# Performance work log

Measured on AMD Instinct MI355X. Metric: run time of the kernel, lower is better.

Reference implementation:

```python
import jax, jax.numpy as jnp
import numpy as np

H = 2048       # hidden_size
NH = 16        # num query heads
NKV = 4        # num key/value heads
HD = 128       # head_dim
EPS = 1e-6
ROPE_BASE = 10000.0


def rms_norm(x, w):
    xf = x.astype(jnp.float32)
    var = jnp.mean(xf * xf, axis=-1, keepdims=True)
    return (w * (xf * jax.lax.rsqrt(var + EPS)).astype(x.dtype))


def rope_cos_sin(seq_len, dtype):
    inv_freq = 1.0 / (ROPE_BASE ** (jnp.arange(0, HD, 2, dtype=jnp.float32) / HD))
    pos = jnp.arange(seq_len, dtype=jnp.float32)
    ang = pos[:, None] * inv_freq[None, :]            # [S, HD/2]
    emb = jnp.concatenate([ang, ang], axis=-1)        # [S, HD]
    return jnp.cos(emb).astype(dtype), jnp.sin(emb).astype(dtype)


def rotate_half(x):
    x1, x2 = jnp.split(x, 2, axis=-1)
    return jnp.concatenate([-x2, x1], axis=-1)


def setup_inputs() -> dict:
    key = jax.random.key(0)
    ks = jax.random.split(key, 8)
    B, S = 2, 2048
    hidden_states = jax.random.normal(ks[0], (B, S, H), dtype=jnp.float32)
    # additive causal mask [B,1,S,S]
    causal = jnp.where(jnp.tril(jnp.ones((S, S), dtype=bool)), 0.0, -1e9).astype(jnp.float32)
    attention_mask = jnp.broadcast_to(causal[None, None], (B, 1, S, S))
    sc = 1.0 / np.sqrt(H)
    Wq = jax.random.normal(ks[1], (NH * HD, H), dtype=jnp.float32) * sc
    Wk = jax.random.normal(ks[2], (NKV * HD, H), dtype=jnp.float32) * sc
    Wv = jax.random.normal(ks[3], (NKV * HD, H), dtype=jnp.float32) * sc
    Wo = jax.random.normal(ks[4], (H, NH * HD), dtype=jnp.float32) * sc
    q_norm_w = jnp.ones((HD,), dtype=jnp.float32)
    k_norm_w = jnp.ones((HD,), dtype=jnp.float32)
    return {"hidden_states": hidden_states, "attention_mask": attention_mask,
            "Wq": Wq, "Wk": Wk, "Wv": Wv, "Wo": Wo,
            "q_norm_w": q_norm_w, "k_norm_w": k_norm_w}


def reference(hidden_states, attention_mask, Wq, Wk, Wv, Wo, q_norm_w, k_norm_w):
    B, S, _ = hidden_states.shape
    # projections (nn.Linear: x @ W.T)
    q = (hidden_states @ Wq.T).reshape(B, S, NH, HD).transpose(0, 2, 1, 3)   # [B,NH,S,HD]
    k = (hidden_states @ Wk.T).reshape(B, S, NKV, HD).transpose(0, 2, 1, 3)  # [B,NKV,S,HD]
    v = (hidden_states @ Wv.T).reshape(B, S, NKV, HD).transpose(0, 2, 1, 3)
    # QK RMSNorm over head_dim
    q = rms_norm(q, q_norm_w)
    k = rms_norm(k, k_norm_w)
    # RoPE
    cos, sin = rope_cos_sin(S, q.dtype)        # [S,HD]
    q = q * cos + rotate_half(q) * sin
    k = k * cos + rotate_half(k) * sin
    # GQA: repeat kv heads
    n_rep = NH // NKV
    k = jnp.repeat(k, n_rep, axis=1)           # [B,NH,S,HD]
    v = jnp.repeat(v, n_rep, axis=1)
    # attention
    scores = jnp.einsum('bhqd,bhkd->bhqk', q, k) / np.sqrt(HD)
    scores = scores + attention_mask
    probs = jax.nn.softmax(scores, axis=-1)
    attn = jnp.einsum('bhqk,bhkd->bhqd', probs, v)
    attn = attn.transpose(0, 2, 1, 3).reshape(B, S, NH * HD)
    return attn @ Wo.T
```

## Files before the change

kernel.cpp:

```cpp
#include <hip/hip_runtime.h>
#include <hip/hip_bf16.h>
#include <math.h>

#define NH 16
#define NKV 4
#define HD 128
#define SEQ 2048
#define BATCH 2
#define EPSF 1e-6f
#define QKV 3072

typedef __attribute__((ext_vector_type(8))) short bf16x8;
typedef __attribute__((ext_vector_type(4))) short short4v;
typedef __attribute__((ext_vector_type(4))) float f32x4;

__device__ __forceinline__ short f2bf(float x) {
    unsigned u = __float_as_uint(x);
    u += 0x7fffu + ((u >> 16) & 1u);
    return (short)(u >> 16);
}
__device__ __forceinline__ float bf2f(short x) {
    return __uint_as_float((unsigned)(unsigned short)x << 16);
}
__device__ __forceinline__ unsigned pkbf(float a, float b) {
    __hip_bfloat162 h = __float22bfloat162_rn(float2{a, b});
    unsigned r; __builtin_memcpy(&r, &h, 4); return r;
}

__device__ __forceinline__ void gll16(const short* g, short* l) {
    __builtin_amdgcn_global_load_lds(
        (const __attribute__((address_space(1))) unsigned*)g,
        (__attribute__((address_space(3))) unsigned*)l, 16, 0, 0);
}

__global__ __launch_bounds__(256)
void cast_all(const float* __restrict__ hs, const float* __restrict__ Wq,
              const float* __restrict__ Wk, const float* __restrict__ Wv,
              const float* __restrict__ Wo, short* __restrict__ hsb,
              short* __restrict__ wqkv, short* __restrict__ wob)
{
    const size_t MEG = 1024 * 1024;
    const int id = blockIdx.x;
    const float* s;
    short* d;
    size_t off;
    if (id < 8192)       { s = hs; d = hsb;            off = (size_t)id * 1024; }
    else if (id < 12288) { s = Wq; d = wqkv;           off = (size_t)(id - 8192) * 1024; }
    else if (id < 13312) { s = Wk; d = wqkv + 4 * MEG; off = (size_t)(id - 12288) * 1024; }
    else if (id < 14336) { s = Wv; d = wqkv + 5 * MEG; off = (size_t)(id - 13312) * 1024; }
    else                 { s = Wo; d = wob;            off = (size_t)(id - 14336) * 1024; }
    const size_t i = off + threadIdx.x * 4;
    float4 v = *(const float4*)(s + i);
    short4v o;
    o.x = f2bf(v.x); o.y = f2bf(v.y); o.z = f2bf(v.z); o.w = f2bf(v.w);
    *(short4v*)(d + i) = o;
}

template<bool OUT_BF16>
__global__ __launch_bounds__(256)
void gemm_nt_mfma(const short* __restrict__ A, const short* __restrict__ B,
                  void* __restrict__ Cv, int M, int N, int K)
{
    __shared__ short As[128 * 32];
    __shared__ short Bs[128 * 32];

    const int tid = threadIdx.x;
    const int w = tid >> 6, lane = tid & 63;
    const int quad = lane >> 4, ln = lane & 15;
    const int mw = (w >> 1) * 64, nw = (w & 1) * 64;
    const int m0 = blockIdx.y * 128, n0 = blockIdx.x * 128;

    const int srow = w * 16 + (lane >> 2);
    const int scol = (lane & 3) * 8;
    const short* Ag0 = A + (size_t)(m0 + srow) * K + scol;
    const short* Ag1 = Ag0 + (size_t)64 * K;
    const short* Bg0 = B + (size_t)(n0 + srow) * K + scol;
    const short* Bg1 = Bg0 + (size_t)64 * K;
    short* Al0 = &As[(w * 16) * 32];
    short* Al1 = &As[(w * 16 + 64) * 32];
    short* Bl0 = &Bs[(w * 16) * 32];
    short* Bl1 = &Bs[(w * 16 + 64) * 32];

    f32x4 acc[4][4];
    #pragma unroll
    for (int i = 0; i < 4; ++i)
        #pragma unroll
        for (int j = 0; j < 4; ++j)
            acc[i][j] = (f32x4){0.f, 0.f, 0.f, 0.f};

    for (int k0 = 0; k0 < K; k0 += 32) {
        __syncthreads();
        gll16(Ag0 + k0, Al0);
        gll16(Ag1 + k0, Al1);
        gll16(Bg0 + k0, Bl0);
        gll16(Bg1 + k0, Bl1);
        __syncthreads();

        bf16x8 af[4], bfr[4];
        #pragma unroll
        for (int i = 0; i < 4; ++i)
            af[i] = *(const bf16x8*)&As[(mw + i * 16 + ln) * 32 + quad * 8];
        #pragma unroll
        for (int j = 0; j < 4; ++j)
            bfr[j] = *(const bf16x8*)&Bs[(nw + j * 16 + ln) * 32 + quad * 8];
        #pragma unroll
        for (int i = 0; i < 4; ++i)
            #pragma unroll
            for (int j = 0; j < 4; ++j)
                acc[i][j] = __builtin_amdgcn_mfma_f32_16x16x32_bf16(
                    af[i], bfr[j], acc[i][j], 0, 0, 0);
    }

    #pragma unroll
    for (int i = 0; i < 4; ++i) {
        #pragma unroll
        for (int reg = 0; reg < 4; ++reg) {
            const int row = m0 + mw + i * 16 + quad * 4 + reg;
            const size_t base = (size_t)row * N + n0 + nw;
            #pragma unroll
            for (int j = 0; j < 4; ++j) {
                if (OUT_BF16)
                    ((short*)Cv)[base + j * 16 + ln] = f2bf(acc[i][j][reg]);
                else
                    ((float*)Cv)[base + j * 16 + ln] = acc[i][j][reg];
            }
        }
    }
}

__global__ __launch_bounds__(256)
void norm_rope_bf16(short* __restrict__ qkv, const float* __restrict__ qw,
                    const float* __restrict__ kw)
{
    const int wave = threadIdx.x >> 6;
    const int lane = threadIdx.x & 63;
    const long vec = (long)blockIdx.x * 4 + wave;
    const long NQ = (long)BATCH * SEQ * NH;

    short* base;
    const float* w;
    int s;
    if (vec < NQ) {
        const long token = vec / NH;
        const int h = (int)(vec % NH);
        s = (int)(token % SEQ);
        base = qkv + token * QKV + h * HD;
        w = qw;
    } else {
        const long t = vec - NQ;
        const long token = t / NKV;
        const int kvh = (int)(t % NKV);
        s = (int)(token % SEQ);
        base = qkv + token * QKV + 2048 + kvh * HD;
        w = kw;
    }

    float x0 = bf2f(base[lane]);
    float x1 = bf2f(base[lane + 64]);
    float ss = x0 * x0 + x1 * x1;
    #pragma unroll
    for (int off = 32; off; off >>= 1) ss += __shfl_xor(ss, off, 64);
    const float r = rsqrtf(ss * (1.0f / HD) + EPSF);
    x0 = x0 * r * w[lane];
    x1 = x1 * r * w[lane + 64];

    const float inv_freq = expf(-(float)lane * (logf(10000.0f) / 64.0f));
    const float ang = (float)s * inv_freq;
    const float c = cosf(ang);
    const float sn = sinf(ang);
    base[lane]      = f2bf(x0 * c - x1 * sn);
    base[lane + 64] = f2bf(x1 * c + x0 * sn);
}

__global__ __launch_bounds__(256)
void transpose_v(const short* __restrict__ qkv, short* __restrict__ vT)
{
    __shared__ short T[32][33];
    const int bx = blockIdx.x;
    const int st = bx & 63;
    const int dt = (bx >> 6) & 3;
    const int bk = bx >> 8;
    const int s0 = st * 32, d0 = dt * 32;
    const int tid = threadIdx.x;
    const long tok0 = (long)(bk >> 2) * SEQ + s0;
    const int kvh = bk & 3;

    const int rs = tid >> 3;
    const int rc = (tid & 7) * 4;
    short4v val = *(const short4v*)(qkv + (tok0 + rs) * QKV + 2560 + kvh * HD + d0 + rc);
    T[rc + 0][rs] = val.x; T[rc + 1][rs] = val.y;
    T[rc + 2][rs] = val.z; T[rc + 3][rs] = val.w;
    __syncthreads();

    const int wd = tid >> 3;
    const int wsc = (tid & 7) * 4;
    short4v ov;
    ov.x = T[wd][wsc + 0]; ov.y = T[wd][wsc + 1];
    ov.z = T[wd][wsc + 2]; ov.w = T[wd][wsc + 3];
    *(short4v*)(vT + ((size_t)bk * HD + d0 + wd) * SEQ + s0 + wsc) = ov;
}

__global__ __launch_bounds__(512, 4)
void flash_attn_mfma(const short* __restrict__ qkv, const short* __restrict__ vT,
                     short* __restrict__ o)
{
    __shared__ short Ks[64][144];
    __shared__ short Vt[128][80];
    __shared__ short Ps[8][16][80];

    const int tid = threadIdx.x;
    const int w = tid >> 6;
    const int lane = tid & 63;
    const int quad = lane >> 4;
    const int ln = lane & 15;
    const int side = w >> 2;
    const int sw = w & 3;

    const int bx = blockIdx.x;
    const int pair = bx & 15;
    const int bh = bx >> 4;
    const int h = bh & 15;
    const int b = bh >> 4;
    const int kvh = h >> 2;
    const int qa = pair, qb = 31 - pair;
    const int qX = side ? qb : qa;
    const int rX = qX * 64 + sw * 16;

    const float SC = 0.08838834764831845f * 1.4426950408889634f;

    bf16x8 qf[4];
    {
        const short* qrow = qkv + (size_t)(b * SEQ + rX + ln) * QKV + h * HD;
        #pragma unroll
        for (int f = 0; f < 4; ++f)
            qf[f] = *(const bf16x8*)(qrow + f * 32 + quad * 8);
    }

    f32x4 Oa[8];
    #pragma unroll
    for (int dg = 0; dg < 8; ++dg) Oa[dg] = (f32x4){0.f, 0.f, 0.f, 0.f};
    float mX = -1e30f, lX = 0.f;

    const short* kbase = qkv + (size_t)(b * SEQ) * QKV + 2048 + kvh * HD;
    const short* vbase = vT + (size_t)(b * NKV + kvh) * HD * SEQ;

    bf16x8 kp[2], vp[2];
    auto prefetch = [&](int k0) {
        #pragma unroll
        for (int i = 0; i < 2; ++i) {
            const int e = tid + i * 512;
            kp[i] = *(const bf16x8*)(kbase + (size_t)(k0 + (e >> 4)) * QKV + (e & 15) * 8);
            vp[i] = *(const bf16x8*)(vbase + (size_t)(e >> 3) * SEQ + k0 + (e & 7) * 8);
        }
    };
    prefetch(0);

    for (int kt = 0; kt <= qb; ++kt) {
        const int k0 = kt * 64;
        __syncthreads();
        #pragma unroll
        for (int i = 0; i < 2; ++i) {
            const int e = tid + i * 512;
            *(bf16x8*)&Ks[e >> 4][(e & 15) * 8] = kp[i];
            *(bf16x8*)&Vt[e >> 3][(e & 7) * 8] = vp[i];
        }
        __syncthreads();
        if (kt < qb) prefetch(k0 + 64);

        if (kt <= qX) {
            f32x4 s[4];
            #pragma unroll
            for (int g = 0; g < 4; ++g) {
                f32x4 acc = (f32x4){0.f, 0.f, 0.f, 0.f};
                #pragma unroll
                for (int f = 0; f < 4; ++f) {
                    bf16x8 kf = *(const bf16x8*)&Ks[g * 16 + ln][f * 32 + quad * 8];
                    acc = __builtin_amdgcn_mfma_f32_16x16x32_bf16(kf, qf[f], acc, 0, 0, 0);
                }
                s[g] = acc;
            }
            if (kt == qX) {
                const int qrow = rX + ln;
                #pragma unroll
                for (int g = 0; g < 4; ++g)
                    #pragma unroll
                    for (int reg = 0; reg < 4; ++reg) {
                        const int key = k0 + g * 16 + quad * 4 + reg;
                        if (key > qrow) s[g][reg] = -1e30f;
                    }
            }
            float mt = s[0][0];
            #pragma unroll
            for (int g = 0; g < 4; ++g)
                #pragma unroll
                for (int reg = 0; reg < 4; ++reg)
                    mt = fmaxf(mt, s[g][reg]);
            mt = fmaxf(mt, __shfl_xor(mt, 16, 64));
            mt = fmaxf(mt, __shfl_xor(mt, 32, 64));
            const float mnew = fmaxf(mX, mt);
            const float c1 = SC * mnew;
            const float alpha = exp2f(__builtin_fmaf(SC, mX, -c1));
            float ps = 0.f;
            #pragma unroll
            for (int g = 0; g < 4; ++g) {
                float p0 = exp2f(__builtin_fmaf(s[g][0], SC, -c1));
                float p1 = exp2f(__builtin_fmaf(s[g][1], SC, -c1));
                float p2 = exp2f(__builtin_fmaf(s[g][2], SC, -c1));
                float p3 = exp2f(__builtin_fmaf(s[g][3], SC, -c1));
                ps += (p0 + p1) + (p2 + p3);
                uint2 pk;
                pk.x = pkbf(p0, p1);
                pk.y = pkbf(p2, p3);
                *(uint2*)&Ps[w][ln][g * 16 + quad * 4] = pk;
            }
            ps += __shfl_xor(ps, 16, 64);
            ps += __shfl_xor(ps, 32, 64);
            lX = lX * alpha + ps;
            mX = mnew;
            #pragma unroll
            for (int dg = 0; dg < 8; ++dg) {
                Oa[dg][0] *= alpha; Oa[dg][1] *= alpha;
                Oa[dg][2] *= alpha; Oa[dg][3] *= alpha;
            }
            __asm volatile("s_waitcnt lgkmcnt(0)" ::: "memory");
            bf16x8 pf0 = *(const bf16x8*)&Ps[w][ln][quad * 8];
            bf16x8 pf1 = *(const bf16x8*)&Ps[w][ln][32 + quad * 8];
            #pragma unroll
            for (int dg = 0; dg < 8; ++dg) {
                bf16x8 vf0 = *(const bf16x8*)&Vt[dg * 16 + ln][quad * 8];
                bf16x8 vf1 = *(const bf16x8*)&Vt[dg * 16 + ln][32 + quad * 8];
                Oa[dg] = __builtin_amdgcn_mfma_f32_16x16x32_bf16(vf0, pf0, Oa[dg], 0, 0, 0);
                Oa[dg] = __builtin_amdgcn_mfma_f32_16x16x32_bf16(vf1, pf1, Oa[dg], 0, 0, 0);
            }
        }
    }

    {
        const float inv = 1.0f / lX;
        short* orow = o + ((size_t)(b * SEQ + rX + ln) * NH + h) * HD;
        #pragma unroll
        for (int dg = 0; dg < 8; ++dg) {
            uint2 ov;
            ov.x = pkbf(Oa[dg][0] * inv, Oa[dg][1] * inv);
            ov.y = pkbf(Oa[dg][2] * inv, Oa[dg][3] * inv);
            *(uint2*)(orow + dg * 16 + quad * 4) = ov;
        }
    }
}

extern "C" void kernel_launch(void* const* d_in, const int* in_sizes, int n_in,
                              void* d_out, int out_size, void* d_ws, size_t ws_size,
                              hipStream_t stream)
{
    const float* hs = (const float*)d_in[0];
    const float* Wq = (const float*)d_in[2];
    const float* Wk = (const float*)d_in[3];
    const float* Wv = (const float*)d_in[4];
    const float* Wo = (const float*)d_in[5];
    const float* qw = (const float*)d_in[6];
    const float* kw = (const float*)d_in[7];
    float* out = (float*)d_out;

    const size_t MEG = 1024 * 1024;
    short* hsb  = (short*)d_ws;
    short* wqkv = hsb + 8 * MEG;
    short* wob  = wqkv + 6 * MEG;
    short* qkvb = wob + 4 * MEG;
    short* vT   = (short*)d_out;

    const int M = BATCH * SEQ;
    dim3 blk(256);

    cast_all<<<dim3(18432), blk, 0, stream>>>(hs, Wq, Wk, Wv, Wo, hsb, wqkv, wob);

    gemm_nt_mfma<true><<<dim3(QKV / 128, M / 128), blk, 0, stream>>>(
        hsb, wqkv, qkvb, M, QKV, 2048);

    norm_rope_bf16<<<dim3((BATCH * SEQ * (NH + NKV)) / 4), blk, 0, stream>>>(
        qkvb, qw, kw);

    transpose_v<<<dim3(2048), blk, 0, stream>>>(qkvb, vT);

    flash_attn_mfma<<<dim3(512), dim3(512), 0, stream>>>(qkvb, vT, hsb);

    gemm_nt_mfma<false><<<dim3(2048 / 128, M / 128), blk, 0, stream>>>(
        hsb, wob, out, M, 2048, 2048);
}
```

Before: 358.4 us.

## Deepen GEMM K-tile to 64 with XOR-swizzled LDS and XCD-aware block remap

The GEMM kernel now loads 64-wide K slices per iteration instead of 32, halving the number of barrier pairs, and applies an XOR swizzle on global-to-LDS columns to avoid LDS bank conflicts on fragment reads. Blocks are launched on a 1D grid and remapped so consecutive tiles land on the same XCD (id&7 interleave), improving L2 locality on the multi-die GPU. Launch bounds request 3 blocks per SM. LDS usage doubles, which may limit occupancy.

New measurement: 330.0 us. 1.09x faster.

```diff
diff --git a/kernel.cpp b/kernel.cpp
--- a/kernel.cpp
+++ b/kernel.cpp
@@ -57,29 +57,38 @@
 }
 
 template<bool OUT_BF16>
-__global__ __launch_bounds__(256)
+__global__ __launch_bounds__(256, 3)
 void gemm_nt_mfma(const short* __restrict__ A, const short* __restrict__ B,
-                  void* __restrict__ Cv, int M, int N, int K)
-{
-    __shared__ short As[128 * 32];
-    __shared__ short Bs[128 * 32];
+                  void* __restrict__ Cv, int N, int K, int gridX, int total)
+{
+    __shared__ short As[128 * 64];
+    __shared__ short Bs[128 * 64];
 
     const int tid = threadIdx.x;
     const int w = tid >> 6, lane = tid & 63;
     const int quad = lane >> 4, ln = lane & 15;
     const int mw = (w >> 1) * 64, nw = (w & 1) * 64;
-    const int m0 = blockIdx.y * 128, n0 = blockIdx.x * 128;
-
-    const int srow = w * 16 + (lane >> 2);
-    const int scol = (lane & 3) * 8;
-    const short* Ag0 = A + (size_t)(m0 + srow) * K + scol;
-    const short* Ag1 = Ag0 + (size_t)64 * K;
-    const short* Bg0 = B + (size_t)(n0 + srow) * K + scol;
-    const short* Bg1 = Bg0 + (size_t)64 * K;
-    short* Al0 = &As[(w * 16) * 32];
-    short* Al1 = &As[(w * 16 + 64) * 32];
-    short* Bl0 = &Bs[(w * 16) * 32];
-    short* Bl1 = &Bs[(w * 16 + 64) * 32];
+
+    const int id = blockIdx.x;
+    const int t = (id & 7) * (total >> 3) + (id >> 3);
+    const int n0 = (t % gridX) * 128;
+    const int m0 = (t / gridX) * 128;
+
+    const int rr = lane >> 3;
+    const int gsw = ((lane & 7) ^ rr) * 8;
+    const short* Ag[4]; const short* Bg[4];
+    short* Al[4]; short* Bl[4];
+    #pragma unroll
+    for (int r = 0; r < 4; ++r) {
+        const int row = w * 8 + 32 * r + rr;
+        Ag[r] = A + (size_t)(m0 + row) * K + gsw;
+        Bg[r] = B + (size_t)(n0 + row) * K + gsw;
+        Al[r] = &As[(w * 8 + 32 * r) * 64];
+        Bl[r] = &Bs[(w * 8 + 32 * r) * 64];
+    }
+
+    const int col0 = ((quad) ^ (ln & 7)) * 8;
+    const int col1 = ((4 + quad) ^ (ln & 7)) * 8;
 
     f32x4 acc[4][4];
     #pragma unroll
@@ -88,27 +97,32 @@
         for (int j = 0; j < 4; ++j)
             acc[i][j] = (f32x4){0.f, 0.f, 0.f, 0.f};
 
-    for (int k0 = 0; k0 < K; k0 += 32) {
+    for (int k0 = 0; k0 < K; k0 += 64) {
         __syncthreads();
-        gll16(Ag0 + k0, Al0);
-        gll16(Ag1 + k0, Al1);
-        gll16(Bg0 + k0, Bl0);
-        gll16(Bg1 + k0, Bl1);
+        #pragma unroll
+        for (int r = 0; r < 4; ++r) {
+            gll16(Ag[r] + k0, Al[r]);
+            gll16(Bg[r] + k0, Bl[r]);
+        }
         __syncthreads();
 
-        bf16x8 af[4], bfr[4];
-        #pragma unroll
-        for (int i = 0; i < 4; ++i)
-            af[i] = *(const bf16x8*)&As[(mw + i * 16 + ln) * 32 + quad * 8];
-        #pragma unroll
-        for (int j = 0; j < 4; ++j)
-            bfr[j] = *(const bf16x8*)&Bs[(nw + j * 16 + ln) * 32 + quad * 8];
-        #pragma unroll
-        for (int i = 0; i < 4; ++i)
+        #pragma unroll
+        for (int ks = 0; ks < 2; ++ks) {
+            const int col = ks ? col1 : col0;
+            bf16x8 af[4], bfr[4];
+            #pragma unroll
+            for (int i = 0; i < 4; ++i)
+                af[i] = *(const bf16x8*)&As[(mw + i * 16 + ln) * 64 + col];
             #pragma unroll
             for (int j = 0; j < 4; ++j)
-                acc[i][j] = __builtin_amdgcn_mfma_f32_16x16x32_bf16(
-                    af[i], bfr[j], acc[i][j], 0, 0, 0);
+                bfr[j] = *(const bf16x8*)&Bs[(nw + j * 16 + ln) * 64 + col];
+            #pragma unroll
+            for (int i = 0; i < 4; ++i)
+                #pragma unroll
+                for (int j = 0; j < 4; ++j)
+                    acc[i][j] = __builtin_amdgcn_mfma_f32_16x16x32_bf16(
+                        af[i], bfr[j], acc[i][j], 0, 0, 0);
+        }
     }
 
     #pragma unroll
@@ -368,13 +382,12 @@
     short* qkvb = wob + 4 * MEG;
     short* vT   = (short*)d_out;
 
-    const int M = BATCH * SEQ;
     dim3 blk(256);
 
     cast_all<<<dim3(18432), blk, 0, stream>>>(hs, Wq, Wk, Wv, Wo, hsb, wqkv, wob);
 
-    gemm_nt_mfma<true><<<dim3(QKV / 128, M / 128), blk, 0, stream>>>(
-        hsb, wqkv, qkvb, M, QKV, 2048);
+    gemm_nt_mfma<true><<<dim3(768), blk, 0, stream>>>(
+        hsb, wqkv, qkvb, QKV, 2048, 24, 768);
 
     norm_rope_bf16<<<dim3((BATCH * SEQ * (NH + NKV)) / 4), blk, 0, stream>>>(
         qkvb, qw, kw);
@@ -383,6 +396,6 @@
 
     flash_attn_mfma<<<dim3(512), dim3(512), 0, stream>>>(qkvb, vT, hsb);
 
-    gemm_nt_mfma<false><<<dim3(2048 / 128, M / 128), blk, 0, stream>>>(
-        hsb, wob, out, M, 2048, 2048);
-}
+    gemm_nt_mfma<false><<<dim3(512), blk, 0, stream>>>(
+        hsb, wob, out, 2048, 2048, 16, 512);
+}
```
